# Optimization experiments

Hardware: AMD Instinct MI355X
Metric: run time of the kernel (lower is better)

## Reference

```python
import jax, jax.numpy as jnp
import numpy as np

K = 3      # kernel size (hardcoded 3x3 in the torch module via repeat(...,9,...))
PAD = 1
STRIDE = 1


def _unfold(x):
    # torch.nn.functional.unfold equivalent: (B,C,H,W) -> (B,C,K,K,oh,ow)
    B, C, H, W = x.shape
    p = jax.lax.conv_general_dilated_patches(
        x, (K, K), (STRIDE, STRIDE), ((PAD, PAD), (PAD, PAD)))
    oh, ow = p.shape[2], p.shape[3]
    return p.reshape(B, C, K, K, oh, ow)


def setup_inputs() -> dict:
    key = jax.random.key(0)
    k1, k2, k3, k4 = jax.random.split(key, 4)
    B, Cin, Cout, H, W = 4, 64, 64, 128, 128
    inputs = jax.random.normal(k1, (B, Cin, H, W), jnp.float32)
    depth = jax.random.uniform(k2, (B, 1, H, W), jnp.float32)  # positive depths
    weight = jax.random.uniform(k3, (K, Cout, Cin, K, K), jnp.float32, minval=-0.05, maxval=0.05)
    bias = jax.random.uniform(k4, (Cout,), jnp.float32, minval=-0.05, maxval=0.05)
    return {"inputs": inputs, "depth": depth, "weight": weight, "bias": bias, "f": 1}


def reference(inputs, depth, weight, bias, f):
    # --- DepthKernelFn: per-depth-plane binary masks ---
    depth_wins = _unfold(depth)          # (B,1,K,K,oh,ow)
    s_wins = depth_wins / f              # grid spacing s_i = d / f
    cy, cx = K // 2, K // 2
    d0 = depth_wins[:, :, cy, cx]        # center depth      (B,1,oh,ow)
    s0 = s_wins[:, :, cy, cx]            # center spacing    (B,1,oh,ow)
    offs = jnp.arange(K, dtype=inputs.dtype) - (K - 1) / 2.0  # l - (K-1)/2
    # z_l at center: d0 + (l-1)*s0  -> (K,B,1,oh,ow)
    z0 = d0[None] + offs[:, None, None, None, None] * s0[None]
    half = s0[None] / 2
    a = (z0 - half)[:, :, :, None, None]  # (K,B,1,1,1,oh,ow)
    b = (z0 + half)[:, :, :, None, None]
    dw = depth_wins[None]                 # (1,B,1,K,K,oh,ow)
    # mask_l = 1 where a <= depth < b else 0  (same as the where-cascade in torch)
    mask = ((dw >= a) & (dw < b)).astype(inputs.dtype)  # (K,B,1,K,K,oh,ow)

    # --- RepeatKernelConvFn: masked windowed conv via einsum ---
    inp_wins = _unfold(inputs)            # (B,C,K,K,oh,ow)
    x = inp_wins[None] * mask             # (K,B,C,K,K,oh,ow), depth C=1 broadcasts
    out = jnp.einsum('hijklmn,hojkl->iomn', x, weight)
    out = out + bias.reshape(1, -1, 1, 1)
    return out
```

## Files before the change

kernel.cpp:

```cpp
#include <hip/hip_runtime.h>
#include <math.h>

#define B_N  4
#define CIN  64
#define COUT 64
#define H_N  128
#define W_N  128

typedef _Float16 half8 __attribute__((ext_vector_type(8)));
typedef float    f32x4 __attribute__((ext_vector_type(4)));

#define KTOT   1728
#define NSTEP  54
#define WA_BYTES ((size_t)NSTEP * 4 * 64 * 8 * 2)

__global__ void wprep(const float* __restrict__ w, _Float16* __restrict__ wa) {
    int idx = blockIdx.x * 256 + threadIdx.x;
    if (idx >= NSTEP * 4 * 64) return;
    int lane = idx & 63;
    int mt   = (idx >> 6) & 3;
    int s    = idx >> 8;
    int m    = mt * 16 + (lane & 15);
    int kl0  = (lane >> 4) * 8;
    _Float16 v[8];
#pragma unroll
    for (int j = 0; j < 8; ++j) {
        int k = s * 32 + kl0 + j;
        int g = k >> 6;
        int c = k & 63;
        int t = g / 3;
        int h = g % 3;
        v[j] = (_Float16)w[(((size_t)(h * COUT) + m) * CIN + c) * 9 + t];
    }
    *(int4*)&wa[(size_t)idx * 8] = *(int4*)v;
}

#define XS_LINE 64
#define XS_ROW  (130 * XS_LINE)

__global__ __launch_bounds__(256, 2)
void conv_mfma(const float* __restrict__ inp, const float* __restrict__ depth,
               const _Float16* __restrict__ wa, const float* __restrict__ bias,
               const int* __restrict__ fptr, float* __restrict__ out) {
    __shared__ _Float16 Xs[3 * XS_ROW];
    __shared__ unsigned hLds[128];

    int bid  = blockIdx.x;
    int y    = bid & (H_N - 1);
    int b    = bid >> 7;
    int tid  = threadIdx.x;
    int lane = tid & 63;
    int mq   = tid >> 6;
    int ln15 = lane & 15;
    int quad = lane >> 4;

    int xl    = tid & 127;
    int chalf = tid >> 7;
    int xi    = xl + 1;
    int key   = xi & 7;

    const size_t HW = (size_t)H_N * W_N;

#define LOAD_ROW(dyi, buf) {                                                  \
        int yy_ = y + (dyi) - 1;                                              \
        if (yy_ >= 0 && yy_ < H_N) {                                          \
            const float* src_ = inp + (((size_t)b * CIN + chalf * 32) * H_N + yy_) * W_N + xl; \
            _Pragma("unroll")                                                 \
            for (int cc = 0; cc < 32; ++cc) buf[cc] = src_[(size_t)cc * HW];  \
        } else {                                                              \
            _Pragma("unroll")                                                 \
            for (int cc = 0; cc < 32; ++cc) buf[cc] = 0.f;                    \
        }                                                                     \
    }

#define WRITE_ROW(dyi, buf) {                                                 \
        _Float16 hb_[32];                                                     \
        _Pragma("unroll")                                                     \
        for (int cc = 0; cc < 32; ++cc) hb_[cc] = (_Float16)buf[cc];          \
        _Float16* dst_ = &Xs[(dyi) * XS_ROW + xi * XS_LINE];                  \
        _Pragma("unroll")                                                     \
        for (int k = 0; k < 4; ++k)                                           \
            *(int4*)&dst_[((chalf * 4 + k) ^ key) * 8] = *(int4*)&hb_[k * 8]; \
    }

    const half8* wa8 = (const half8*)wa;
    half8 Abuf[2][6];

    float rbuf[32];
    LOAD_ROW(0, rbuf);

    {
        const half8* bA = wa8 + (size_t)mq * 64 + lane;
#pragma unroll
        for (int j = 0; j < 6; ++j) Abuf[0][j] = bA[(size_t)j * 4 * 64];
    }

    if (tid < 48) {
        int dyi = tid / 16;
        int rem = tid % 16;
        int xz  = (rem >= 8) ? 129 : 0;
        int k8  = rem & 7;
        int4 z  = {0, 0, 0, 0};
        *(int4*)&Xs[dyi * XS_ROW + xz * XS_LINE + k8 * 8] = z;
    }

    if (tid < 128) {
        int x = tid;
        double fd  = (double)(*fptr);
        float  d0f = depth[((size_t)b * H_N + y) * W_N + x];
        double dd  = (double)d0f;
        double inv = fd / dd;
        bool   pos = (inv > 0.0);
        unsigned pk = 0;
        for (int t = 0; t < 9; ++t) {
            int dy = t / 3 - 1, dx = t % 3 - 1;
            int yy = y + dy, xx = x + dx;
            float dwf = (yy >= 0 && yy < H_N && xx >= 0 && xx < W_N)
                        ? depth[((size_t)b * H_N + yy) * W_N + xx] : 0.f;
            int h = -1;
            if (pos) {
                double u  = ((double)dwf - dd) * inv + 1.5;
                double uf = floor(u);
                if (uf >= 0.0 && uf <= 2.0) h = (int)uf;
            }
            pk |= (unsigned)(h + 1) << (2 * t);
        }
        hLds[tid] = pk;
    }

    WRITE_ROW(0, rbuf);
    __syncthreads();

    unsigned hpk[8];
#pragma unroll
    for (int nt = 0; nt < 8; ++nt) hpk[nt] = hLds[nt * 16 + ln15];

    f32x4 acc[8];
#pragma unroll
    for (int nt = 0; nt < 8; ++nt) acc[nt] = (f32x4){0.f, 0.f, 0.f, 0.f};

    half8 z8 = {(_Float16)0.f, (_Float16)0.f, (_Float16)0.f, (_Float16)0.f,
                (_Float16)0.f, (_Float16)0.f, (_Float16)0.f, (_Float16)0.f};

#pragma unroll
    for (int r = 0; r < 3; ++r) {
        float nbuf[32];
        if (r < 2) LOAD_ROW(r + 1, nbuf);

#pragma unroll
        for (int dxl = 0; dxl < 3; ++dxl) {
            int t  = r * 3 + dxl;
            int dx = dxl - 1;

            half8 bb[16];
#pragma unroll
            for (int nt = 0; nt < 8; ++nt) {
                int xs = nt * 16 + ln15 + dx + 1;
                int k2 = xs & 7;
                int ba = r * XS_ROW + xs * XS_LINE;
                bb[nt * 2 + 0] = *(const half8*)&Xs[ba + ((quad    ) ^ k2) * 8];
                bb[nt * 2 + 1] = *(const half8*)&Xs[ba + ((quad + 4) ^ k2) * 8];
            }

            if (t < 8) {
                const half8* bA = wa8 + ((size_t)(t + 1) * 24 + mq) * 64 + lane;
#pragma unroll
                for (int j = 0; j < 6; ++j) Abuf[(t + 1) & 1][j] = bA[(size_t)j * 4 * 64];
            }

            int hb[8];
#pragma unroll
            for (int nt = 0; nt < 8; ++nt) hb[nt] = (hpk[nt] >> (2 * t)) & 3;

#pragma unroll
            for (int h = 0; h < 3; ++h) {
#pragma unroll
                for (int kk = 0; kk < 2; ++kk) {
                    int j = h * 2 + kk;
#pragma unroll
                    for (int nt = 0; nt < 8; ++nt) {
                        half8 c = (hb[nt] == h + 1) ? bb[nt * 2 + kk] : z8;
                        acc[nt] = __builtin_amdgcn_mfma_f32_16x16x32_f16(Abuf[t & 1][j], c, acc[nt], 0, 0, 0);
                    }
                }
            }
        }

        if (r < 2) {
            WRITE_ROW(r + 1, nbuf);
            __syncthreads();
        }
    }
#undef LOAD_ROW
#undef WRITE_ROW

#pragma unroll
    for (int nt = 0; nt < 8; ++nt) {
        int x = nt * 16 + ln15;
#pragma unroll
        for (int rr = 0; rr < 4; ++rr) {
            int o = mq * 16 + quad * 4 + rr;
            out[(((size_t)b * COUT + o) * H_N + y) * W_N + x] = acc[nt][rr] + bias[o];
        }
    }
}

__global__ __launch_bounds__(256)
void conv25d(const float* __restrict__ inp, const float* __restrict__ depth,
             const float* __restrict__ wsrc, const float* __restrict__ bias,
             const int* __restrict__ fptr, float* __restrict__ out) {
    int bid = blockIdx.x;
    int xt  = bid & 3;
    int y   = (bid >> 2) & (H_N - 1);
    int b   = bid >> 9;
    int o   = threadIdx.x & 63;
    int q   = threadIdx.x >> 6;
    int x0  = xt * 32 + q * 8;
    double fd = (double)(*fptr);
    float acc[8];
    float bv = bias[o];
#pragma unroll
    for (int i = 0; i < 8; ++i) acc[i] = bv;
    const float* dcen = depth + ((size_t)b * H_N + y) * W_N;
    float d0[8];
#pragma unroll
    for (int i = 0; i < 8; ++i) d0[i] = dcen[x0 + i];
    for (int t = 0; t < 9; ++t) {
        int dy = t / 3 - 1, dx = t % 3 - 1;
        int yy = y + dy;
        if (yy < 0 || yy >= H_N) continue;
        const float* drow = depth + ((size_t)b * H_N + yy) * W_N;
        int hsel[8];
#pragma unroll
        for (int i = 0; i < 8; ++i) {
            int xx = x0 + i + dx;
            int h = -1;
            if (xx >= 0 && xx < W_N) {
                double dd = (double)d0[i];
                double s0 = dd / fd;
                if (s0 > 0.0) {
                    double u = ((double)drow[xx] - dd) / s0 + 1.5;
                    double uf = floor(u);
                    if (uf >= 0.0 && uf <= 2.0) h = (int)uf;
                }
            }
            hsel[i] = h;
        }
        const float* irow = inp + ((size_t)b * CIN * H_N + yy) * W_N;
        for (int c = 0; c < CIN; ++c) {
            const float* wb = wsrc + ((size_t)o * CIN + c) * 9 + t;
            float w0 = wb[0], w1 = wb[(size_t)COUT * CIN * 9], w2 = wb[2 * (size_t)COUT * CIN * 9];
            const float* ir = irow + (size_t)c * H_N * W_N;
#pragma unroll
            for (int i = 0; i < 8; ++i) {
                int h = hsel[i];
                if (h >= 0) {
                    float wv = (h == 0) ? w0 : ((h == 1) ? w1 : w2);
                    acc[i] = fmaf(ir[x0 + i + dx], wv, acc[i]);
                }
            }
        }
    }
    float* orow = out + (((size_t)b * COUT + o) * H_N + y) * W_N;
#pragma unroll
    for (int i = 0; i < 8; ++i) orow[x0 + i] = acc[i];
}

extern "C" void kernel_launch(void* const* d_in, const int* in_sizes, int n_in,
                              void* d_out, int out_size, void* d_ws, size_t ws_size,
                              hipStream_t stream) {
    const float* inp   = (const float*)d_in[0];
    const float* depth = (const float*)d_in[1];
    const float* w     = (const float*)d_in[2];
    const float* bias  = (const float*)d_in[3];
    const int*   f     = (const int*)d_in[4];
    float* out = (float*)d_out;

    if (ws_size >= WA_BYTES) {
        _Float16* wa = (_Float16*)d_ws;
        wprep<<<NSTEP, 256, 0, stream>>>(w, wa);
        conv_mfma<<<B_N * H_N, 256, 0, stream>>>(inp, depth, wa, bias, f, out);
    } else {
        conv25d<<<B_N * H_N * (W_N / 32), 256, 0, stream>>>(inp, depth, w, bias, f, out);
    }
}
```

Baseline: 96.65 us.

## Ping-pong two LDS row planes and raise occupancy to three blocks per CU

Shrinks the shared input tile from three row planes to two, alternating between them. The row-r+1 tile is written into the plane that finished being read before the previous barrier. Operand fragments are now loaded in two groups of four column tiles instead of all eight at once, which cuts live registers. Together with `__launch_bounds__(256, 3)`, this aims to fit three blocks per CU, trading a tighter register budget (risk of spills) for more latency hiding.

```diff
diff --git a/kernel.cpp b/kernel.cpp
--- a/kernel.cpp
+++ b/kernel.cpp
@@ -35,14 +35,14 @@
     *(int4*)&wa[(size_t)idx * 8] = *(int4*)v;
 }
 
-#define XS_LINE 64
-#define XS_ROW  (130 * XS_LINE)
-
-__global__ __launch_bounds__(256, 2)
+#define XS_LINE  64
+#define XS_PLANE (130 * XS_LINE)
+
+__global__ __launch_bounds__(256, 3)
 void conv_mfma(const float* __restrict__ inp, const float* __restrict__ depth,
                const _Float16* __restrict__ wa, const float* __restrict__ bias,
                const int* __restrict__ fptr, float* __restrict__ out) {
-    __shared__ _Float16 Xs[3 * XS_ROW];
+    __shared__ _Float16 Xs[2 * XS_PLANE];
     __shared__ unsigned hLds[128];
 
     int bid  = blockIdx.x;
@@ -73,11 +73,11 @@
         }                                                                     \
     }
 
-#define WRITE_ROW(dyi, buf) {                                                 \
+#define WRITE_ROW(pl, buf) {                                                  \
         _Float16 hb_[32];                                                     \
         _Pragma("unroll")                                                     \
         for (int cc = 0; cc < 32; ++cc) hb_[cc] = (_Float16)buf[cc];          \
-        _Float16* dst_ = &Xs[(dyi) * XS_ROW + xi * XS_LINE];                  \
+        _Float16* dst_ = &Xs[(pl) * XS_PLANE + xi * XS_LINE];                 \
         _Pragma("unroll")                                                     \
         for (int k = 0; k < 4; ++k)                                           \
             *(int4*)&dst_[((chalf * 4 + k) ^ key) * 8] = *(int4*)&hb_[k * 8]; \
@@ -95,13 +95,13 @@
         for (int j = 0; j < 6; ++j) Abuf[0][j] = bA[(size_t)j * 4 * 64];
     }
 
-    if (tid < 48) {
-        int dyi = tid / 16;
-        int rem = tid % 16;
+    if (tid < 32) {
+        int pl  = tid >> 4;
+        int rem = tid & 15;
         int xz  = (rem >= 8) ? 129 : 0;
         int k8  = rem & 7;
         int4 z  = {0, 0, 0, 0};
-        *(int4*)&Xs[dyi * XS_ROW + xz * XS_LINE + k8 * 8] = z;
+        *(int4*)&Xs[pl * XS_PLANE + xz * XS_LINE + k8 * 8] = z;
     }
 
     if (tid < 128) {
@@ -144,6 +144,8 @@
 
 #pragma unroll
     for (int r = 0; r < 3; ++r) {
+        int pr = r & 1;
+
         float nbuf[32];
         if (r < 2) LOAD_ROW(r + 1, nbuf);
 
@@ -152,42 +154,43 @@
             int t  = r * 3 + dxl;
             int dx = dxl - 1;
 
-            half8 bb[16];
-#pragma unroll
-            for (int nt = 0; nt < 8; ++nt) {
-                int xs = nt * 16 + ln15 + dx + 1;
-                int k2 = xs & 7;
-                int ba = r * XS_ROW + xs * XS_LINE;
-                bb[nt * 2 + 0] = *(const half8*)&Xs[ba + ((quad    ) ^ k2) * 8];
-                bb[nt * 2 + 1] = *(const half8*)&Xs[ba + ((quad + 4) ^ k2) * 8];
-            }
-
             if (t < 8) {
                 const half8* bA = wa8 + ((size_t)(t + 1) * 24 + mq) * 64 + lane;
 #pragma unroll
                 for (int j = 0; j < 6; ++j) Abuf[(t + 1) & 1][j] = bA[(size_t)j * 4 * 64];
             }
 
-            int hb[8];
-#pragma unroll
-            for (int nt = 0; nt < 8; ++nt) hb[nt] = (hpk[nt] >> (2 * t)) & 3;
-
-#pragma unroll
-            for (int h = 0; h < 3; ++h) {
-#pragma unroll
-                for (int kk = 0; kk < 2; ++kk) {
-                    int j = h * 2 + kk;
-#pragma unroll
-                    for (int nt = 0; nt < 8; ++nt) {
-                        half8 c = (hb[nt] == h + 1) ? bb[nt * 2 + kk] : z8;
-                        acc[nt] = __builtin_amdgcn_mfma_f32_16x16x32_f16(Abuf[t & 1][j], c, acc[nt], 0, 0, 0);
+#pragma unroll
+            for (int g = 0; g < 2; ++g) {
+                half8 bb[8];
+#pragma unroll
+                for (int ntl = 0; ntl < 4; ++ntl) {
+                    int nt = g * 4 + ntl;
+                    int xs = nt * 16 + ln15 + dx + 1;
+                    int k2 = xs & 7;
+                    int ba = pr * XS_PLANE + xs * XS_LINE;
+                    bb[ntl * 2 + 0] = *(const half8*)&Xs[ba + ((quad    ) ^ k2) * 8];
+                    bb[ntl * 2 + 1] = *(const half8*)&Xs[ba + ((quad + 4) ^ k2) * 8];
+                }
+#pragma unroll
+                for (int h = 0; h < 3; ++h) {
+#pragma unroll
+                    for (int kk = 0; kk < 2; ++kk) {
+                        int j = h * 2 + kk;
+#pragma unroll
+                        for (int ntl = 0; ntl < 4; ++ntl) {
+                            int nt = g * 4 + ntl;
+                            int hb = (hpk[nt] >> (2 * t)) & 3;
+                            half8 c = (hb == h + 1) ? bb[ntl * 2 + kk] : z8;
+                            acc[nt] = __builtin_amdgcn_mfma_f32_16x16x32_f16(Abuf[t & 1][j], c, acc[nt], 0, 0, 0);
+                        }
                     }
                 }
             }
         }
 
         if (r < 2) {
-            WRITE_ROW(r + 1, nbuf);
+            WRITE_ROW((r + 1) & 1, nbuf);
             __syncthreads();
         }
     }
```

Result: slower. 101.4 us (+4.9%).
